# Kernel optimization log

Measured on AMD Instinct MI355X. Metric: run time of the kernel, lower is better.

## Reference

```python
import jax, jax.numpy as jnp
import numpy as np

N_NODES = 50000
N_EDGES = 800000
D_IN = 64
D_OUT = 64


def setup_inputs() -> dict:
    key = jax.random.key(0)
    k1, k2, k3, k4 = jax.random.split(key, 4)
    x = jax.random.normal(k1, (N_NODES, D_IN), dtype=jnp.float32)
    edge_index = jax.random.randint(k2, (2, N_EDGES), 0, N_NODES, dtype=jnp.int64)
    W = jax.random.normal(k3, (D_IN, D_OUT), dtype=jnp.float32) * (1.0 / np.sqrt(D_IN))
    b = jax.random.normal(k4, (D_OUT,), dtype=jnp.float32) * 0.01
    return {"x": x, "edge_index": edge_index, "W": W, "b": b}


def reference(x, edge_index, W, b):
    N = x.shape[0]
    # Add self-loops (PyG GCNConv default add_self_loops=True)
    loop = jnp.arange(N, dtype=edge_index.dtype)
    src = jnp.concatenate([edge_index[0], loop])  # source j
    dst = jnp.concatenate([edge_index[1], loop])  # target i
    # Linear transform first (standard GCNConv: theta then propagate)
    xw = x @ W  # [N, D_OUT]
    # Symmetric degree normalization: deg over targets of (A + I)
    ones = jnp.ones(src.shape[0], dtype=x.dtype)
    deg = jax.ops.segment_sum(ones, dst, num_segments=N)
    dis = jnp.where(deg > 0, jax.lax.rsqrt(jnp.maximum(deg, 1.0)), 0.0)
    norm = dis[src] * dis[dst]  # [E+N]
    # Gather, weight, scatter-add
    msgs = norm[:, None] * xw[src]  # [E+N, D_OUT]
    out = jax.ops.segment_sum(msgs, dst, num_segments=N) + b
    return jax.nn.relu(out)
```

## Files before the change

### kernel.cpp

```cpp
#include <hip/hip_runtime.h>

#define N_NODES 50000
#define N_EDGES 800000
#define D 64
#define FINE_SHIFT 6
#define NBUCK 782
#define CAP 1280
#define SEGCAP 64
#define EPB 8192
#define NPART 98
#define NMM 196
#define NSTART (NBUCK + 1)

typedef _Float16 f16;
typedef __attribute__((ext_vector_type(4))) _Float16 f16x4;
typedef __attribute__((ext_vector_type(8))) _Float16 f16x8;
typedef __attribute__((ext_vector_type(4))) float f32x4;

#define SMEM_PART (2 * NBUCK * 4 + EPB * 4)
#define SMEM_MM   (64 * 72 * 2 + 256 * 72 * 2)
#define SMEM_SZ   (SMEM_MM > SMEM_PART ? SMEM_MM : SMEM_PART)

__global__ __launch_bounds__(1024) void partition_matmul(
    const int* __restrict__ src, const int* __restrict__ dst,
    unsigned int* __restrict__ binned2, int* __restrict__ starts2,
    const float* __restrict__ W, const float* __restrict__ x,
    f16* __restrict__ xwh)
{
    __shared__ __align__(16) unsigned char smem[SMEM_SZ];
    int tid = threadIdx.x;

    if (blockIdx.x >= NPART) {
        f16 (*WtH)[72]  = (f16 (*)[72])smem;
        f16 (*park)[72] = (f16 (*)[72])(smem + 64 * 72 * 2);

        for (int j = tid; j < 4096; j += 1024)
            WtH[j & 63][j >> 6] = (f16)W[j];
        __syncthreads();

        int nb = (blockIdx.x - NPART) * 256;
        int wave = tid >> 6, lane = tid & 63;
        int m = lane & 15, q = lane >> 4;

        int ar = nb + wave * 16 + m;
        if (ar >= N_NODES) ar = N_NODES - 1;
        const float4* x4 = (const float4*)x;
        size_t rb = (size_t)ar * 16;
        float4 p0 = x4[rb + q * 2];
        float4 p1 = x4[rb + q * 2 + 1];
        float4 p2 = x4[rb + 8 + q * 2];
        float4 p3 = x4[rb + 8 + q * 2 + 1];
        f16x8 a0 = { (f16)p0.x, (f16)p0.y, (f16)p0.z, (f16)p0.w,
                     (f16)p1.x, (f16)p1.y, (f16)p1.z, (f16)p1.w };
        f16x8 a1 = { (f16)p2.x, (f16)p2.y, (f16)p2.z, (f16)p2.w,
                     (f16)p3.x, (f16)p3.y, (f16)p3.z, (f16)p3.w };

        f32x4 acc[4];
        #pragma unroll
        for (int t = 0; t < 4; ++t) {
            int n0 = t * 16;
            f16x8 b0 = *(const f16x8*)&WtH[n0 + m][q * 8];
            f16x8 b1 = *(const f16x8*)&WtH[n0 + m][32 + q * 8];
            f32x4 z = { 0.f, 0.f, 0.f, 0.f };
            z = __builtin_amdgcn_mfma_f32_16x16x32_f16(a0, b0, z, 0, 0, 0);
            acc[t] = __builtin_amdgcn_mfma_f32_16x16x32_f16(a1, b1, z, 0, 0, 0);
        }

        #pragma unroll
        for (int t = 0; t < 4; ++t) {
            int n0 = t * 16;
            #pragma unroll
            for (int r = 0; r < 4; ++r)
                park[wave * 16 + q * 4 + r][n0 + m] = (f16)acc[t][r];
        }
        __syncthreads();

        for (int j = tid; j < 2048; j += 1024) {
            int row = j >> 3, seg = (j & 7) * 8;
            int n = nb + row;
            if (n < N_NODES)
                *(f16x8*)&xwh[(size_t)n * D + seg] = *(const f16x8*)&park[row][seg];
        }
        return;
    }

    int* hist            = (int*)smem;
    int* start_s         = hist + NBUCK;
    unsigned int* staged = (unsigned int*)(start_s + NBUCK);

    int eb  = blockIdx.x * EPB;
    int total = N_EDGES - eb; if (total > EPB) total = EPB;

    for (int i = tid; i < NBUCK; i += 1024) hist[i] = 0;
    __syncthreads();

    unsigned int rec[8];
    int rank[8];
    int jb = tid * 8;
    if (jb < total) {
        int4 s0 = *(const int4*)&src[eb + jb];
        int4 s1 = *(const int4*)&src[eb + jb + 4];
        int4 d0 = *(const int4*)&dst[eb + jb];
        int4 d1 = *(const int4*)&dst[eb + jb + 4];
        rec[0] = ((unsigned)d0.x << 16) | (unsigned)s0.x;
        rec[1] = ((unsigned)d0.y << 16) | (unsigned)s0.y;
        rec[2] = ((unsigned)d0.z << 16) | (unsigned)s0.z;
        rec[3] = ((unsigned)d0.w << 16) | (unsigned)s0.w;
        rec[4] = ((unsigned)d1.x << 16) | (unsigned)s1.x;
        rec[5] = ((unsigned)d1.y << 16) | (unsigned)s1.y;
        rec[6] = ((unsigned)d1.z << 16) | (unsigned)s1.z;
        rec[7] = ((unsigned)d1.w << 16) | (unsigned)s1.w;
        #pragma unroll
        for (int u = 0; u < 8; ++u)
            rank[u] = atomicAdd(&hist[rec[u] >> (16 + FINE_SHIFT)], 1);
    } else {
        #pragma unroll
        for (int u = 0; u < 8; ++u) rec[u] = 0xFFFFFFFFu;
    }
    __syncthreads();

    if (tid < 64) {
        int b0 = tid * 13;
        int v[13]; int run = 0;
        #pragma unroll
        for (int j = 0; j < 13; ++j) {
            int idx = b0 + j;
            int c = (idx < NBUCK) ? hist[idx] : 0;
            v[j] = run; run += c;
        }
        int s = run;
        #pragma unroll
        for (int off = 1; off < 64; off <<= 1) {
            int t = __shfl_up(s, off);
            if (tid >= off) s += t;
        }
        int excl = s - run;
        #pragma unroll
        for (int j = 0; j < 13; ++j) {
            int idx = b0 + j;
            if (idx < NBUCK) start_s[idx] = excl + v[j];
        }
    }
    __syncthreads();

    #pragma unroll
    for (int u = 0; u < 8; ++u) {
        unsigned int v = rec[u];
        if (v != 0xFFFFFFFFu)
            staged[start_s[v >> 22] + rank[u]] = v;
    }
    __syncthreads();

    for (int i = tid; i < total; i += 1024)
        binned2[(size_t)blockIdx.x * EPB + i] = staged[i];
    for (int i = tid; i < NBUCK; i += 1024)
        starts2[(size_t)blockIdx.x * NSTART + i] = start_s[i];
    if (tid == 0)
        starts2[(size_t)blockIdx.x * NSTART + NBUCK] = total;
}

__global__ __launch_bounds__(512) void compact_degree(
    const unsigned int* __restrict__ binned2, const int* __restrict__ starts2,
    unsigned int* __restrict__ binned, int* __restrict__ cntc,
    float* __restrict__ dis)
{
    __shared__ int segcnt_s[NPART], segbase_s[NPART], segsrc_s[NPART];
    __shared__ int segoff_s[NPART];
    __shared__ int h[64];
    __shared__ int stot_s;

    int cb = blockIdx.x, tid = threadIdx.x;
    if (tid < 64) h[tid] = 0;
    if (tid < NPART) {
        int base = tid * NSTART + cb;
        int s0 = starts2[base], s1 = starts2[base + 1];
        int c = s1 - s0; if (c < 0) c = 0; if (c > SEGCAP) c = SEGCAP;
        segoff_s[tid] = s0; segcnt_s[tid] = c;
    }
    __syncthreads();

    if (tid < 64) {
        int v0 = segcnt_s[tid], s = v0;
        #pragma unroll
        for (int off = 1; off < 64; off <<= 1) {
            int t = __shfl_up(s, off);
            if (tid >= off) s += t;
        }
        segbase_s[tid] = s - v0;
        int T0 = __shfl(s, 63);
        int v1 = (tid < NPART - 64) ? segcnt_s[64 + tid] : 0;
        int s1 = v1;
        #pragma unroll
        for (int off = 1; off < 64; off <<= 1) {
            int t = __shfl_up(s1, off);
            if (tid >= off) s1 += t;
        }
        if (tid < NPART - 64) segbase_s[64 + tid] = T0 + s1 - v1;
        int T1 = __shfl(s1, 63);
        if (tid == 0) {
            int tot = T0 + T1; if (tot > CAP) tot = CAP;
            stot_s = tot;
        }
    }
    __syncthreads();
    if (tid < NPART)
        segsrc_s[tid] = tid * EPB + segoff_s[tid] - segbase_s[tid];
    __syncthreads();

    int stot = stot_s;
    for (int i = tid; i < stot; i += 512) {
        int lo = 0, hi = NPART - 1;
        #pragma unroll
        for (int it = 0; it < 7; ++it) {
            int mid = (lo + hi + 1) >> 1;
            if (segbase_s[mid] <= i) lo = mid; else hi = mid - 1;
        }
        unsigned int r = binned2[segsrc_s[lo] + i];
        binned[(size_t)cb * CAP + i] = r;
        atomicAdd(&h[(r >> 16) & 63], 1);
    }
    __syncthreads();

    if (tid == 0) cntc[cb] = stot;
    int n = cb * 64 + tid;
    if (tid < 64 && n < N_NODES)
        dis[n] = rsqrtf((float)h[tid] + 1.0f);
}

__global__ __launch_bounds__(512) void gather_out(
    const int* __restrict__ cntc, const unsigned int* __restrict__ binned,
    const f16* __restrict__ xwh, const float* __restrict__ dis,
    const float* __restrict__ b, float* __restrict__ out)
{
    __shared__ unsigned short ssrc[CAP];
    __shared__ int h[64], off_s[64], cur[64];

    int cb = blockIdx.x, tid = threadIdx.x;
    int wave = tid >> 6, lane = tid & 63;
    int nb = cb * 64;
    int cnt = cntc[cb];
    if (cnt < 0) cnt = 0; if (cnt > CAP) cnt = CAP;
    const unsigned int* br = binned + (size_t)cb * CAP;

    if (tid < 64) h[tid] = 0;
    __syncthreads();

    unsigned int rec[3];
    #pragma unroll
    for (int u = 0; u < 3; ++u) {
        int j = u * 512 + tid;
        if (j < cnt) {
            rec[u] = br[j];
            atomicAdd(&h[(rec[u] >> 16) & 63], 1);
        } else rec[u] = 0xFFFFFFFFu;
    }
    __syncthreads();

    if (tid < 64) {
        int v = h[tid], s = v;
        #pragma unroll
        for (int off = 1; off < 64; off <<= 1) {
            int t = __shfl_up(s, off);
            if (tid >= off) s += t;
        }
        off_s[tid] = s - v;
        cur[tid]   = s - v;
    }
    __syncthreads();

    #pragma unroll
    for (int u = 0; u < 3; ++u) {
        unsigned int v = rec[u];
        if (v != 0xFFFFFFFFu) {
            int p = atomicAdd(&cur[(v >> 16) & 63], 1);
            ssrc[p] = (unsigned short)(v & 0xFFFFu);
        }
    }
    __syncthreads();

    const f16x4* xw4 = (const f16x4*)xwh;
    const float4* b4p = (const float4*)b;
    float4* out4 = (float4*)out;
    int g = lane >> 4, c16 = lane & 15;

    for (int i = 0; i < 8; ++i) {
        int nl = wave * 8 + i;
        int n  = nb + nl;
        if (n >= N_NODES) break;
        int off = off_s[nl], c = h[nl];
        float dn = rsqrtf((float)c + 1.0f);

        float a0 = 0.f, a1 = 0.f, a2 = 0.f, a3 = 0.f;
        if (g == 0) {
            f16x4 sv = xw4[(size_t)n * 16 + c16];
            a0 = dn * (float)sv.x; a1 = dn * (float)sv.y;
            a2 = dn * (float)sv.z; a3 = dn * (float)sv.w;
        }
        int k = off + g, e = off + c;
        for (; k + 12 < e; k += 16) {
            int s0 = ssrc[k], s1 = ssrc[k + 4], s2 = ssrc[k + 8], s3 = ssrc[k + 12];
            float d0 = dis[s0], d1 = dis[s1], d2 = dis[s2], d3 = dis[s3];
            f16x4 v0 = xw4[(size_t)s0 * 16 + c16];
            f16x4 v1 = xw4[(size_t)s1 * 16 + c16];
            f16x4 v2 = xw4[(size_t)s2 * 16 + c16];
            f16x4 v3 = xw4[(size_t)s3 * 16 + c16];
            a0 = fmaf(d0, (float)v0.x, a0); a1 = fmaf(d0, (float)v0.y, a1);
            a2 = fmaf(d0, (float)v0.z, a2); a3 = fmaf(d0, (float)v0.w, a3);
            a0 = fmaf(d1, (float)v1.x, a0); a1 = fmaf(d1, (float)v1.y, a1);
            a2 = fmaf(d1, (float)v1.z, a2); a3 = fmaf(d1, (float)v1.w, a3);
            a0 = fmaf(d2, (float)v2.x, a0); a1 = fmaf(d2, (float)v2.y, a1);
            a2 = fmaf(d2, (float)v2.z, a2); a3 = fmaf(d2, (float)v2.w, a3);
            a0 = fmaf(d3, (float)v3.x, a0); a1 = fmaf(d3, (float)v3.y, a1);
            a2 = fmaf(d3, (float)v3.z, a2); a3 = fmaf(d3, (float)v3.w, a3);
        }
        for (; k + 4 < e; k += 8) {
            int s0 = ssrc[k], s1 = ssrc[k + 4];
            float d0 = dis[s0], d1 = dis[s1];
            f16x4 v0 = xw4[(size_t)s0 * 16 + c16];
            f16x4 v1 = xw4[(size_t)s1 * 16 + c16];
            a0 = fmaf(d0, (float)v0.x, a0); a1 = fmaf(d0, (float)v0.y, a1);
            a2 = fmaf(d0, (float)v0.z, a2); a3 = fmaf(d0, (float)v0.w, a3);
            a0 = fmaf(d1, (float)v1.x, a0); a1 = fmaf(d1, (float)v1.y, a1);
            a2 = fmaf(d1, (float)v1.z, a2); a3 = fmaf(d1, (float)v1.w, a3);
        }
        if (k < e) {
            int s = ssrc[k];
            float d = dis[s];
            f16x4 v = xw4[(size_t)s * 16 + c16];
            a0 = fmaf(d, (float)v.x, a0); a1 = fmaf(d, (float)v.y, a1);
            a2 = fmaf(d, (float)v.z, a2); a3 = fmaf(d, (float)v.w, a3);
        }
        a0 += __shfl_xor(a0, 32); a1 += __shfl_xor(a1, 32);
        a2 += __shfl_xor(a2, 32); a3 += __shfl_xor(a3, 32);
        a0 += __shfl_xor(a0, 16); a1 += __shfl_xor(a1, 16);
        a2 += __shfl_xor(a2, 16); a3 += __shfl_xor(a3, 16);
        if (g == 0) {
            float4 bl = b4p[c16];
            float4 r;
            r.x = fmaxf(bl.x + dn * a0, 0.f);
            r.y = fmaxf(bl.y + dn * a1, 0.f);
            r.z = fmaxf(bl.z + dn * a2, 0.f);
            r.w = fmaxf(bl.w + dn * a3, 0.f);
            out4[(size_t)n * 16 + c16] = r;
        }
    }
}

extern "C" void kernel_launch(void* const* d_in, const int* in_sizes, int n_in,
                              void* d_out, int out_size, void* d_ws, size_t ws_size,
                              hipStream_t stream) {
    const float* x  = (const float*)d_in[0];
    const int*   ei = (const int*)d_in[1];
    const float* W  = (const float*)d_in[2];
    const float* b  = (const float*)d_in[3];

    const int* src = ei;
    const int* dst = ei + N_EDGES;
    float* out = (float*)d_out;

    f16*          xwh     = (f16*)d_ws;
    unsigned int* binned2 = (unsigned int*)(xwh + (size_t)N_NODES * D);
    int*          starts2 = (int*)(binned2 + (size_t)NPART * EPB);
    unsigned int* binned  = (unsigned int*)(starts2 + (size_t)NPART * NSTART);
    int*          cntc    = (int*)(binned + (size_t)NBUCK * CAP);
    float*        dis     = (float*)(cntc + NBUCK);

    partition_matmul<<<NPART + NMM, 1024, 0, stream>>>(
        src, dst, binned2, starts2, W, x, xwh);
    compact_degree<<<NBUCK, 512, 0, stream>>>(binned2, starts2, binned, cntc, dis);
    gather_out<<<NBUCK, 512, 0, stream>>>(cntc, binned, xwh, dis, b, out);
}
```

Measured before the change: 106.6 us.

## Pre-scale xw rows by source degree and gather straight from partitioned buckets

The degree kernel no longer writes a compacted edge list, count array or dis array. Instead it scales each node's fp16 xw row in place by its inverse square-root degree. The gather kernel rebuilds the segment offsets itself and reads edges directly from the partition output, and its inner loop becomes a plain sum with no per-edge dis lookups. This removes one global write and read pass and the random dis gathers. In exchange the segment scan and binary search are repeated in the gather kernel, and the pre-scaled values take an extra fp16 rounding.

```diff
diff --git a/kernel.cpp b/kernel.cpp
--- a/kernel.cpp
+++ b/kernel.cpp
@@ -159,13 +159,11 @@
         starts2[(size_t)blockIdx.x * NSTART + NBUCK] = total;
 }
 
-__global__ __launch_bounds__(512) void compact_degree(
+__global__ __launch_bounds__(256) void degree_scale(
     const unsigned int* __restrict__ binned2, const int* __restrict__ starts2,
-    unsigned int* __restrict__ binned, int* __restrict__ cntc,
-    float* __restrict__ dis)
+    f16* __restrict__ xwh)
 {
     __shared__ int segcnt_s[NPART], segbase_s[NPART], segsrc_s[NPART];
-    __shared__ int segoff_s[NPART];
     __shared__ int h[64];
     __shared__ int stot_s;
 
@@ -175,7 +173,8 @@
         int base = tid * NSTART + cb;
         int s0 = starts2[base], s1 = starts2[base + 1];
         int c = s1 - s0; if (c < 0) c = 0; if (c > SEGCAP) c = SEGCAP;
-        segoff_s[tid] = s0; segcnt_s[tid] = c;
+        segcnt_s[tid] = c;
+        segsrc_s[tid] = tid * EPB + s0;
     }
     __syncthreads();
 
@@ -203,12 +202,11 @@
         }
     }
     __syncthreads();
-    if (tid < NPART)
-        segsrc_s[tid] = tid * EPB + segoff_s[tid] - segbase_s[tid];
+    if (tid < NPART) segsrc_s[tid] -= segbase_s[tid];
     __syncthreads();
 
     int stot = stot_s;
-    for (int i = tid; i < stot; i += 512) {
+    for (int i = tid; i < stot; i += 256) {
         int lo = 0, hi = NPART - 1;
         #pragma unroll
         for (int it = 0; it < 7; ++it) {
@@ -216,41 +214,89 @@
             if (segbase_s[mid] <= i) lo = mid; else hi = mid - 1;
         }
         unsigned int r = binned2[segsrc_s[lo] + i];
-        binned[(size_t)cb * CAP + i] = r;
         atomicAdd(&h[(r >> 16) & 63], 1);
     }
     __syncthreads();
 
-    if (tid == 0) cntc[cb] = stot;
-    int n = cb * 64 + tid;
-    if (tid < 64 && n < N_NODES)
-        dis[n] = rsqrtf((float)h[tid] + 1.0f);
+    int nb = cb * 64;
+    for (int j = tid; j < 512; j += 256) {
+        int row = j >> 3, seg = (j & 7) * 8;
+        int n = nb + row;
+        if (n < N_NODES) {
+            float dn = rsqrtf((float)h[row] + 1.0f);
+            f16x8 v = *(f16x8*)&xwh[(size_t)n * D + seg];
+            #pragma unroll
+            for (int e = 0; e < 8; ++e)
+                v[e] = (f16)((float)v[e] * dn);
+            *(f16x8*)&xwh[(size_t)n * D + seg] = v;
+        }
+    }
 }
 
 __global__ __launch_bounds__(512) void gather_out(
-    const int* __restrict__ cntc, const unsigned int* __restrict__ binned,
-    const f16* __restrict__ xwh, const float* __restrict__ dis,
-    const float* __restrict__ b, float* __restrict__ out)
+    const unsigned int* __restrict__ binned2, const int* __restrict__ starts2,
+    const f16* __restrict__ xwh, const float* __restrict__ b,
+    float* __restrict__ out)
 {
     __shared__ unsigned short ssrc[CAP];
     __shared__ int h[64], off_s[64], cur[64];
+    __shared__ int segcnt_s[NPART], segbase_s[NPART], segsrc_s[NPART];
+    __shared__ int stot_s;
 
     int cb = blockIdx.x, tid = threadIdx.x;
     int wave = tid >> 6, lane = tid & 63;
     int nb = cb * 64;
-    int cnt = cntc[cb];
-    if (cnt < 0) cnt = 0; if (cnt > CAP) cnt = CAP;
-    const unsigned int* br = binned + (size_t)cb * CAP;
 
     if (tid < 64) h[tid] = 0;
-    __syncthreads();
-
+    if (tid < NPART) {
+        int base = tid * NSTART + cb;
+        int s0 = starts2[base], s1 = starts2[base + 1];
+        int c = s1 - s0; if (c < 0) c = 0; if (c > SEGCAP) c = SEGCAP;
+        segcnt_s[tid] = c;
+        segsrc_s[tid] = tid * EPB + s0;
+    }
+    __syncthreads();
+
+    if (tid < 64) {
+        int v0 = segcnt_s[tid], s = v0;
+        #pragma unroll
+        for (int off = 1; off < 64; off <<= 1) {
+            int t = __shfl_up(s, off);
+            if (tid >= off) s += t;
+        }
+        segbase_s[tid] = s - v0;
+        int T0 = __shfl(s, 63);
+        int v1 = (tid < NPART - 64) ? segcnt_s[64 + tid] : 0;
+        int s1 = v1;
+        #pragma unroll
+        for (int off = 1; off < 64; off <<= 1) {
+            int t = __shfl_up(s1, off);
+            if (tid >= off) s1 += t;
+        }
+        if (tid < NPART - 64) segbase_s[64 + tid] = T0 + s1 - v1;
+        int T1 = __shfl(s1, 63);
+        if (tid == 0) {
+            int tot = T0 + T1; if (tot > CAP) tot = CAP;
+            stot_s = tot;
+        }
+    }
+    __syncthreads();
+    if (tid < NPART) segsrc_s[tid] -= segbase_s[tid];
+    __syncthreads();
+
+    int cnt = stot_s;
     unsigned int rec[3];
     #pragma unroll
     for (int u = 0; u < 3; ++u) {
         int j = u * 512 + tid;
         if (j < cnt) {
-            rec[u] = br[j];
+            int lo = 0, hi = NPART - 1;
+            #pragma unroll
+            for (int it = 0; it < 7; ++it) {
+                int mid = (lo + hi + 1) >> 1;
+                if (segbase_s[mid] <= j) lo = mid; else hi = mid - 1;
+            }
+            rec[u] = binned2[segsrc_s[lo] + j];
             atomicAdd(&h[(rec[u] >> 16) & 63], 1);
         } else rec[u] = 0xFFFFFFFFu;
     }
@@ -293,42 +339,32 @@
         float a0 = 0.f, a1 = 0.f, a2 = 0.f, a3 = 0.f;
         if (g == 0) {
             f16x4 sv = xw4[(size_t)n * 16 + c16];
-            a0 = dn * (float)sv.x; a1 = dn * (float)sv.y;
-            a2 = dn * (float)sv.z; a3 = dn * (float)sv.w;
+            a0 = (float)sv.x; a1 = (float)sv.y; a2 = (float)sv.z; a3 = (float)sv.w;
         }
         int k = off + g, e = off + c;
         for (; k + 12 < e; k += 16) {
             int s0 = ssrc[k], s1 = ssrc[k + 4], s2 = ssrc[k + 8], s3 = ssrc[k + 12];
-            float d0 = dis[s0], d1 = dis[s1], d2 = dis[s2], d3 = dis[s3];
             f16x4 v0 = xw4[(size_t)s0 * 16 + c16];
             f16x4 v1 = xw4[(size_t)s1 * 16 + c16];
             f16x4 v2 = xw4[(size_t)s2 * 16 + c16];
             f16x4 v3 = xw4[(size_t)s3 * 16 + c16];
-            a0 = fmaf(d0, (float)v0.x, a0); a1 = fmaf(d0, (float)v0.y, a1);
-            a2 = fmaf(d0, (float)v0.z, a2); a3 = fmaf(d0, (float)v0.w, a3);
-            a0 = fmaf(d1, (float)v1.x, a0); a1 = fmaf(d1, (float)v1.y, a1);
-            a2 = fmaf(d1, (float)v1.z, a2); a3 = fmaf(d1, (float)v1.w, a3);
-            a0 = fmaf(d2, (float)v2.x, a0); a1 = fmaf(d2, (float)v2.y, a1);
-            a2 = fmaf(d2, (float)v2.z, a2); a3 = fmaf(d2, (float)v2.w, a3);
-            a0 = fmaf(d3, (float)v3.x, a0); a1 = fmaf(d3, (float)v3.y, a1);
-            a2 = fmaf(d3, (float)v3.z, a2); a3 = fmaf(d3, (float)v3.w, a3);
+            a0 += (float)v0.x + (float)v1.x + (float)v2.x + (float)v3.x;
+            a1 += (float)v0.y + (float)v1.y + (float)v2.y + (float)v3.y;
+            a2 += (float)v0.z + (float)v1.z + (float)v2.z + (float)v3.z;
+            a3 += (float)v0.w + (float)v1.w + (float)v2.w + (float)v3.w;
         }
         for (; k + 4 < e; k += 8) {
             int s0 = ssrc[k], s1 = ssrc[k + 4];
-            float d0 = dis[s0], d1 = dis[s1];
             f16x4 v0 = xw4[(size_t)s0 * 16 + c16];
             f16x4 v1 = xw4[(size_t)s1 * 16 + c16];
-            a0 = fmaf(d0, (float)v0.x, a0); a1 = fmaf(d0, (float)v0.y, a1);
-            a2 = fmaf(d0, (float)v0.z, a2); a3 = fmaf(d0, (float)v0.w, a3);
-            a0 = fmaf(d1, (float)v1.x, a0); a1 = fmaf(d1, (float)v1.y, a1);
-            a2 = fmaf(d1, (float)v1.z, a2); a3 = fmaf(d1, (float)v1.w, a3);
+            a0 += (float)v0.x + (float)v1.x;
+            a1 += (float)v0.y + (float)v1.y;
+            a2 += (float)v0.z + (float)v1.z;
+            a3 += (float)v0.w + (float)v1.w;
         }
         if (k < e) {
-            int s = ssrc[k];
-            float d = dis[s];
-            f16x4 v = xw4[(size_t)s * 16 + c16];
-            a0 = fmaf(d, (float)v.x, a0); a1 = fmaf(d, (float)v.y, a1);
-            a2 = fmaf(d, (float)v.z, a2); a3 = fmaf(d, (float)v.w, a3);
+            f16x4 v = xw4[(size_t)ssrc[k] * 16 + c16];
+            a0 += (float)v.x; a1 += (float)v.y; a2 += (float)v.z; a3 += (float)v.w;
         }
         a0 += __shfl_xor(a0, 32); a1 += __shfl_xor(a1, 32);
         a2 += __shfl_xor(a2, 32); a3 += __shfl_xor(a3, 32);
@@ -361,12 +397,9 @@
     f16*          xwh     = (f16*)d_ws;
     unsigned int* binned2 = (unsigned int*)(xwh + (size_t)N_NODES * D);
     int*          starts2 = (int*)(binned2 + (size_t)NPART * EPB);
-    unsigned int* binned  = (unsigned int*)(starts2 + (size_t)NPART * NSTART);
-    int*          cntc    = (int*)(binned + (size_t)NBUCK * CAP);
-    float*        dis     = (float*)(cntc + NBUCK);
 
     partition_matmul<<<NPART + NMM, 1024, 0, stream>>>(
         src, dst, binned2, starts2, W, x, xwh);
-    compact_degree<<<NBUCK, 512, 0, stream>>>(binned2, starts2, binned, cntc, dis);
-    gather_out<<<NBUCK, 512, 0, stream>>>(cntc, binned, xwh, dis, b, out);
+    degree_scale<<<NBUCK, 256, 0, stream>>>(binned2, starts2, xwh);
+    gather_out<<<NBUCK, 512, 0, stream>>>(binned2, starts2, xwh, b, out);
 }
```

After: 106.1 us. Within noise of the previous version (-0.5%).
